# Optimization experiments

Measured on AMD Instinct MI355X. Metric: run time of the kernel, lower is better.

Reference implementation:

```python
import jax, jax.numpy as jnp
import numpy as np

TEMPERATURE = 1.0
EPS = 1e-12


def _l2_normalize(x, axis):
    # torch F.normalize: x / max(||x||_2, eps)
    n = jnp.sqrt(jnp.sum(x * x, axis=axis, keepdims=True))
    return x / jnp.maximum(n, EPS)


def setup_inputs() -> dict:
    key = jax.random.key(0)
    k1, k2 = jax.random.split(key)
    B, C, H, W = 2, 128, 128, 256
    K = 20
    features = jax.random.normal(k1, (B, C, H, W), dtype=jnp.float32)
    prototypes = jax.random.normal(k2, (K, C), dtype=jnp.float32)
    distance_scale = jnp.ones((1,), dtype=jnp.float32)
    return {"features": features, "prototypes": prototypes, "distance_scale": distance_scale}


def reference(features, prototypes, distance_scale):
    # features: [B, C, H, W] -> transpose(1,3) -> [B, W, H, C]
    f = jnp.transpose(features, (0, 3, 2, 1))
    # torch F.normalize default dim=1: on [B, W, H, C] this is the W axis (faithful)
    fn = _l2_normalize(f, axis=1)
    # prototypes [K, C], normalized along dim=1 (features)
    pn = _l2_normalize(prototypes, axis=1)
    # exact euclidean cdist (donot_use_mm): broadcasted diff [B, W, H, K, C]
    diff = fn[:, :, :, None, :] - pn[None, None, None, :, :]
    dist = jnp.sqrt(jnp.sum(diff * diff, axis=-1))  # [B, W, H, K]
    dist = jnp.abs(distance_scale) * dist
    # transpose(3,1): [B, K, H, W]
    logits = -jnp.transpose(dist, (0, 3, 2, 1))
    return logits / TEMPERATURE
```

## Files before the change

### kernel.cpp

```cpp
#include <hip/hip_runtime.h>
#include <math.h>

#define B 2
#define C 128
#define H 128
#define W 256
#define K 20

__global__ __launch_bounds__(256) void isomax_kernel(
    const float* __restrict__ feats,
    const float* __restrict__ protos,
    const float* __restrict__ dscale,
    float* __restrict__ out)
{
    __shared__ __align__(16) float s_pn[C * K];
    __shared__ float s_rn[C];
    __shared__ float s_rp[K];

    const int tid = threadIdx.x;
    const int bh  = blockIdx.x;
    const int b   = bh / H;
    const int h   = bh % H;

    if (tid < K) {
        float ss = 0.f;
        const float* p = protos + tid * C;
        for (int c = 0; c < C; ++c) { float v = p[c]; ss = fmaf(v, v, ss); }
        s_rp[tid] = 1.0f / fmaxf(sqrtf(ss), 1e-12f);
    }
    __syncthreads();

    for (int i = tid; i < K * C; i += 256) {
        int k = i >> 7;
        int c = i & (C - 1);
        s_pn[c * K + k] = protos[i] * s_rp[k];
    }

    const int wave = tid >> 6;
    const int lane = tid & 63;
    for (int c = wave; c < C; c += 4) {
        const float* row = feats + ((size_t)((b * C + c) * H + h)) * W;
        float4 v = ((const float4*)row)[lane];
        float ss = fmaf(v.x, v.x, fmaf(v.y, v.y, fmaf(v.z, v.z, v.w * v.w)));
        #pragma unroll
        for (int off = 32; off > 0; off >>= 1)
            ss += __shfl_xor(ss, off, 64);
        if (lane == 0) s_rn[c] = 1.0f / fmaxf(sqrtf(ss), 1e-12f);
    }
    __syncthreads();

    float acc[K];
    #pragma unroll
    for (int k = 0; k < K; ++k) acc[k] = 0.f;

    const float* fcol = feats + ((size_t)(b * C) * H + h) * W + tid;
    #pragma unroll 4
    for (int c = 0; c < C; ++c) {
        float v = fcol[(size_t)c * H * W] * s_rn[c];
        const float4* pn4 = (const float4*)(&s_pn[c * K]);
        #pragma unroll
        for (int q = 0; q < 5; ++q) {
            float4 p = pn4[q];
            float d0 = v - p.x; acc[q * 4 + 0] = fmaf(d0, d0, acc[q * 4 + 0]);
            float d1 = v - p.y; acc[q * 4 + 1] = fmaf(d1, d1, acc[q * 4 + 1]);
            float d2 = v - p.z; acc[q * 4 + 2] = fmaf(d2, d2, acc[q * 4 + 2]);
            float d3 = v - p.w; acc[q * 4 + 3] = fmaf(d3, d3, acc[q * 4 + 3]);
        }
    }

    const float scale = fabsf(dscale[0]);
    float* ob = out + ((size_t)(b * K) * H + h) * W + tid;
    #pragma unroll
    for (int k = 0; k < K; ++k) {
        ob[(size_t)k * H * W] = -scale * sqrtf(acc[k]);
    }
}

extern "C" void kernel_launch(void* const* d_in, const int* in_sizes, int n_in,
                              void* d_out, int out_size, void* d_ws, size_t ws_size,
                              hipStream_t stream) {
    const float* feats  = (const float*)d_in[0];
    const float* protos = (const float*)d_in[1];
    const float* dscale = (const float*)d_in[2];
    float* out = (float*)d_out;

    isomax_kernel<<<B * H, 256, 0, stream>>>(feats, protos, dscale, out);
}
```

Before: 106.8 us.

## Split W into halves and channels across waves with shared-memory reduction

Launches twice as many blocks, each of 512 threads covering half the W row. The channel loop is split into four chunks of 32 and the partial distance sums are reduced through shared memory before the sqrt and store. Prototype norms are now computed in parallel with wave shuffles instead of a serial loop over 20 threads. The aim is more parallelism and shorter serial chains on a small grid. The cost is that each block still recomputes the full per-channel row norms (reading all W) and the prototype normalization, plus extra LDS traffic and syncs.

```diff
diff --git a/kernel.cpp b/kernel.cpp
--- a/kernel.cpp
+++ b/kernel.cpp
@@ -6,8 +6,12 @@
 #define H 128
 #define W 256
 #define K 20
+#define NT 512
+#define WTILE 128
+#define NCCH 4
+#define CCH 32
 
-__global__ __launch_bounds__(256) void isomax_kernel(
+__global__ __launch_bounds__(NT, 4) void isomax_kernel(
     const float* __restrict__ feats,
     const float* __restrict__ protos,
     const float* __restrict__ dscale,
@@ -16,29 +20,28 @@
     __shared__ __align__(16) float s_pn[C * K];
     __shared__ float s_rn[C];
     __shared__ float s_rp[K];
+    __shared__ float s_red[NCCH][K][WTILE];
 
-    const int tid = threadIdx.x;
-    const int bh  = blockIdx.x;
-    const int b   = bh / H;
-    const int h   = bh % H;
+    const int tid   = threadIdx.x;
+    const int blk   = blockIdx.x;
+    const int whalf = blk & 1;
+    const int bh    = blk >> 1;
+    const int b     = bh / H;
+    const int h     = bh % H;
+    const int wave  = tid >> 6;
+    const int lane  = tid & 63;
 
-    if (tid < K) {
-        float ss = 0.f;
-        const float* p = protos + tid * C;
-        for (int c = 0; c < C; ++c) { float v = p[c]; ss = fmaf(v, v, ss); }
-        s_rp[tid] = 1.0f / fmaxf(sqrtf(ss), 1e-12f);
-    }
-    __syncthreads();
-
-    for (int i = tid; i < K * C; i += 256) {
-        int k = i >> 7;
-        int c = i & (C - 1);
-        s_pn[c * K + k] = protos[i] * s_rp[k];
+    for (int k = wave; k < K; k += 8) {
+        const float* p = protos + k * C;
+        float v0 = p[lane], v1 = p[lane + 64];
+        float ss = fmaf(v0, v0, v1 * v1);
+        #pragma unroll
+        for (int off = 32; off > 0; off >>= 1)
+            ss += __shfl_xor(ss, off, 64);
+        if (lane == 0) s_rp[k] = 1.0f / fmaxf(sqrtf(ss), 1e-12f);
     }
 
-    const int wave = tid >> 6;
-    const int lane = tid & 63;
-    for (int c = wave; c < C; c += 4) {
+    for (int c = wave; c < C; c += 8) {
         const float* row = feats + ((size_t)((b * C + c) * H + h)) * W;
         float4 v = ((const float4*)row)[lane];
         float ss = fmaf(v.x, v.x, fmaf(v.y, v.y, fmaf(v.z, v.z, v.w * v.w)));
@@ -49,14 +52,27 @@
     }
     __syncthreads();
 
+    for (int i = tid; i < K * C; i += NT) {
+        int k = i >> 7;
+        int c = i & (C - 1);
+        s_pn[c * K + k] = protos[i] * s_rp[k];
+    }
+    __syncthreads();
+
+    const int wl  = tid & (WTILE - 1);
+    const int cch = tid >> 7;
+    const int w   = whalf * WTILE + wl;
+
     float acc[K];
     #pragma unroll
     for (int k = 0; k < K; ++k) acc[k] = 0.f;
 
-    const float* fcol = feats + ((size_t)(b * C) * H + h) * W + tid;
+    const float* fcol = feats + ((size_t)(b * C) * H + h) * W + w;
+    const int c0 = cch * CCH;
     #pragma unroll 4
-    for (int c = 0; c < C; ++c) {
-        float v = fcol[(size_t)c * H * W] * s_rn[c];
+    for (int ci = 0; ci < CCH; ++ci) {
+        const int c = c0 + ci;
+        float v = fcol[(size_t)c * (H * W)] * s_rn[c];
         const float4* pn4 = (const float4*)(&s_pn[c * K]);
         #pragma unroll
         for (int q = 0; q < 5; ++q) {
@@ -68,11 +84,19 @@
         }
     }
 
+    #pragma unroll
+    for (int k = 0; k < K; ++k) s_red[cch][k][wl] = acc[k];
+    __syncthreads();
+
     const float scale = fabsf(dscale[0]);
-    float* ob = out + ((size_t)(b * K) * H + h) * W + tid;
+    const int ow = tid & (WTILE - 1);
+    const int kg = tid >> 7;
+    float* ob = out + ((size_t)(b * K) * H + h) * W + whalf * WTILE + ow;
     #pragma unroll
-    for (int k = 0; k < K; ++k) {
-        ob[(size_t)k * H * W] = -scale * sqrtf(acc[k]);
+    for (int j = 0; j < 5; ++j) {
+        const int k = kg * 5 + j;
+        float s = s_red[0][k][ow] + s_red[1][k][ow] + s_red[2][k][ow] + s_red[3][k][ow];
+        ob[(size_t)k * (H * W)] = -scale * sqrtf(s);
     }
 }
 
@@ -84,5 +108,5 @@
     const float* dscale = (const float*)d_in[2];
     float* out = (float*)d_out;
 
-    isomax_kernel<<<B * H, 256, 0, stream>>>(feats, protos, dscale, out);
+    isomax_kernel<<<B * H * 2, NT, 0, stream>>>(feats, protos, dscale, out);
 }
```

New measurement: 92.83 us. 13.1% less time.

## Split into prep and distance kernels using norm-expansion distance formula

Applied to the files above, without the earlier changes.

Replaces the direct squared-difference distance with the expansion ||v||^2 + ||p||^2 - 2 v·p, so each feature value costs one FMA per prototype plus one for its own norm. Row norms and normalized, regrouped prototypes are computed once in a separate prep kernel and kept in workspace. The distance kernel now splits the prototypes across the four waves (5 per wave) over 64-wide column tiles, so there are four times as many blocks. The costs are an extra launch, a second full read of the features, and cancellation error in the expanded form, which is clamped at zero.

```diff
diff --git a/kernel.cpp b/kernel.cpp
--- a/kernel.cpp
+++ b/kernel.cpp
@@ -6,73 +6,117 @@
 #define H 128
 #define W 256
 #define K 20
+#define HW (H * W)
 
-__global__ __launch_bounds__(256) void isomax_kernel(
-    const float* __restrict__ feats,
-    const float* __restrict__ protos,
-    const float* __restrict__ dscale,
-    float* __restrict__ out)
+__global__ __launch_bounds__(256) void isomax_prep(
+    const float* __restrict__ feats, const float* __restrict__ protos,
+    float* __restrict__ rn_ws, float* __restrict__ pn_ws, float* __restrict__ ppsum_ws)
 {
-    __shared__ __align__(16) float s_pn[C * K];
-    __shared__ float s_rn[C];
-    __shared__ float s_rp[K];
+    const int tid = threadIdx.x, wave = tid >> 6, lane = tid & 63;
+    const int blk = blockIdx.x;
 
-    const int tid = threadIdx.x;
-    const int bh  = blockIdx.x;
-    const int b   = bh / H;
-    const int h   = bh % H;
-
-    if (tid < K) {
-        float ss = 0.f;
-        const float* p = protos + tid * C;
-        for (int c = 0; c < C; ++c) { float v = p[c]; ss = fmaf(v, v, ss); }
-        s_rp[tid] = 1.0f / fmaxf(sqrtf(ss), 1e-12f);
-    }
-    __syncthreads();
-
-    for (int i = tid; i < K * C; i += 256) {
-        int k = i >> 7;
-        int c = i & (C - 1);
-        s_pn[c * K + k] = protos[i] * s_rp[k];
-    }
-
-    const int wave = tid >> 6;
-    const int lane = tid & 63;
-    for (int c = wave; c < C; c += 4) {
-        const float* row = feats + ((size_t)((b * C + c) * H + h)) * W;
-        float4 v = ((const float4*)row)[lane];
+    if (blk < 8192) {
+        const int r = blk * 4 + wave;
+        const float4 v = ((const float4*)(feats + (size_t)r * W))[lane];
         float ss = fmaf(v.x, v.x, fmaf(v.y, v.y, fmaf(v.z, v.z, v.w * v.w)));
         #pragma unroll
-        for (int off = 32; off > 0; off >>= 1)
-            ss += __shfl_xor(ss, off, 64);
-        if (lane == 0) s_rn[c] = 1.0f / fmaxf(sqrtf(ss), 1e-12f);
+        for (int off = 32; off > 0; off >>= 1) ss += __shfl_xor(ss, off, 64);
+        if (lane == 0) {
+            const int h  = r & (H - 1);
+            const int bc = r >> 7;
+            const int c  = bc & (C - 1);
+            const int b  = bc >> 7;
+            rn_ws[(b * H + h) * C + c] = 1.0f / fmaxf(sqrtf(ss), 1e-12f);
+        }
+    } else {
+        __shared__ float s_rp[32];
+        __shared__ float s_pp[32];
+        for (int k = wave; k < K; k += 4) {
+            const float* p = protos + k * C;
+            float a = p[lane], bq = p[lane + 64];
+            float ss = fmaf(a, a, bq * bq);
+            #pragma unroll
+            for (int off = 32; off > 0; off >>= 1) ss += __shfl_xor(ss, off, 64);
+            if (lane == 0) {
+                float n  = sqrtf(ss);
+                float rp = 1.0f / fmaxf(n, 1e-12f);
+                s_rp[k] = rp;
+                float nn = n * rp;
+                s_pp[k] = nn * nn;
+            }
+        }
+        __syncthreads();
+        for (int i = tid; i < C * K; i += 256) {
+            const int kg  = i / 640;
+            const int rem = i - kg * 640;
+            const int c   = rem / 5;
+            const int j   = rem - c * 5;
+            const int k   = kg * 5 + j;
+            pn_ws[i] = protos[k * C + c] * s_rp[k];
+        }
+        if (tid < K) ppsum_ws[tid] = s_pp[tid];
     }
-    __syncthreads();
+}
 
-    float acc[K];
-    #pragma unroll
-    for (int k = 0; k < K; ++k) acc[k] = 0.f;
+__global__ __launch_bounds__(256, 4) void isomax_dist(
+    const float* __restrict__ feats, const float* __restrict__ rn_ws,
+    const float* __restrict__ pn_ws, const float* __restrict__ ppsum_ws,
+    const float* __restrict__ dscale, float* __restrict__ out)
+{
+    const int tid = threadIdx.x;
+    const int kg  = __builtin_amdgcn_readfirstlane(tid >> 6);
+    const int wl  = tid & 63;
+    const int blk = blockIdx.x;
+    const int wt  = blk & 3;
+    const int bh  = blk >> 2;
+    const int b   = bh >> 7;
+    const int h   = bh & 127;
+    const int w   = wt * 64 + wl;
 
-    const float* fcol = feats + ((size_t)(b * C) * H + h) * W + tid;
+    const float* fp = feats + ((size_t)b * C * H + h) * W + w;
+    const float* rn = rn_ws + bh * C;
+    const float* pk = pn_ws + kg * (C * 5);
+
+    float S = 0.f;
+    float dacc[5] = {0.f, 0.f, 0.f, 0.f, 0.f};
+
     #pragma unroll 4
-    for (int c = 0; c < C; ++c) {
-        float v = fcol[(size_t)c * H * W] * s_rn[c];
-        const float4* pn4 = (const float4*)(&s_pn[c * K]);
+    for (int c0 = 0; c0 < C; c0 += 4) {
+        const float4 r4 = *(const float4*)(rn + c0);
+        float pp[20];
+        ((float4*)pp)[0] = *(const float4*)(pk + c0 * 5 + 0);
+        ((float4*)pp)[1] = *(const float4*)(pk + c0 * 5 + 4);
+        ((float4*)pp)[2] = *(const float4*)(pk + c0 * 5 + 8);
+        ((float4*)pp)[3] = *(const float4*)(pk + c0 * 5 + 12);
+        ((float4*)pp)[4] = *(const float4*)(pk + c0 * 5 + 16);
+
+        const float v0 = fp[(size_t)(c0 + 0) * HW] * r4.x;
+        const float v1 = fp[(size_t)(c0 + 1) * HW] * r4.y;
+        const float v2 = fp[(size_t)(c0 + 2) * HW] * r4.z;
+        const float v3 = fp[(size_t)(c0 + 3) * HW] * r4.w;
+        S = fmaf(v0, v0, S);
+        S = fmaf(v1, v1, S);
+        S = fmaf(v2, v2, S);
+        S = fmaf(v3, v3, S);
         #pragma unroll
-        for (int q = 0; q < 5; ++q) {
-            float4 p = pn4[q];
-            float d0 = v - p.x; acc[q * 4 + 0] = fmaf(d0, d0, acc[q * 4 + 0]);
-            float d1 = v - p.y; acc[q * 4 + 1] = fmaf(d1, d1, acc[q * 4 + 1]);
-            float d2 = v - p.z; acc[q * 4 + 2] = fmaf(d2, d2, acc[q * 4 + 2]);
-            float d3 = v - p.w; acc[q * 4 + 3] = fmaf(d3, d3, acc[q * 4 + 3]);
+        for (int j = 0; j < 5; ++j) {
+            float d = dacc[j];
+            d = fmaf(v0, pp[j],      d);
+            d = fmaf(v1, pp[5 + j],  d);
+            d = fmaf(v2, pp[10 + j], d);
+            d = fmaf(v3, pp[15 + j], d);
+            dacc[j] = d;
         }
     }
 
     const float scale = fabsf(dscale[0]);
-    float* ob = out + ((size_t)(b * K) * H + h) * W + tid;
+    const float* pps = ppsum_ws + kg * 5;
+    float* ob = out + ((size_t)b * K * H + h) * W + w;
     #pragma unroll
-    for (int k = 0; k < K; ++k) {
-        ob[(size_t)k * H * W] = -scale * sqrtf(acc[k]);
+    for (int j = 0; j < 5; ++j) {
+        const int k = kg * 5 + j;
+        float dist2 = fmaxf(fmaf(-2.f, dacc[j], S + pps[j]), 0.f);
+        ob[(size_t)k * HW] = -scale * sqrtf(dist2);
     }
 }
 
@@ -84,5 +128,11 @@
     const float* dscale = (const float*)d_in[2];
     float* out = (float*)d_out;
 
-    isomax_kernel<<<B * H, 256, 0, stream>>>(feats, protos, dscale, out);
+    float* rn_ws    = (float*)d_ws;
+    float* pn_ws    = rn_ws + 32768;
+    float* ppsum_ws = pn_ws + 2560;
+
+    isomax_prep<<<8193, 256, 0, stream>>>(feats, protos, rn_ws, pn_ws, ppsum_ws);
+    isomax_dist<<<B * H * (W / 64), 256, 0, stream>>>(feats, rn_ws, pn_ws, ppsum_ws,
+                                                      dscale, out);
 }
```

Result: faster. 96.91 us (-9.3%).

## Compute prototype distances via bf16 MFMA dot products with norm expansion

Applied to the files above, without the earlier changes.

Replaces the per-thread direct squared-difference accumulation with the expansion ||u||^2 + ||p||^2 - 2u·p. The dot products run on 16x16x32 bf16 MFMA instructions, and both norms are computed from the bf16-rounded values so the terms stay consistent. Blocks grow to 1024 threads, with 16 waves each taking 16 columns, and outputs are staged in shared memory for vectorized float4 stores. Quantizing to bf16 and using the expansion can introduce cancellation error and loses precision relative to the exact fp32 cdist.

```diff
diff --git a/kernel.cpp b/kernel.cpp
--- a/kernel.cpp
+++ b/kernel.cpp
@@ -6,73 +6,135 @@
 #define H 128
 #define W 256
 #define K 20
+#define HW (H * W)
+#define SO_STRIDE 260
 
-__global__ __launch_bounds__(256) void isomax_kernel(
-    const float* __restrict__ feats,
-    const float* __restrict__ protos,
-    const float* __restrict__ dscale,
-    float* __restrict__ out)
+typedef float f32x4 __attribute__((ext_vector_type(4)));
+typedef short bf16x8 __attribute__((ext_vector_type(8)));
+
+__device__ __forceinline__ unsigned f2bf_bits(float x) {
+    unsigned u = __float_as_uint(x);
+    return (u + 0x7FFFu + ((u >> 16) & 1u)) >> 16;
+}
+__device__ __forceinline__ float bf_to_f(unsigned bits) {
+    return __uint_as_float(bits << 16);
+}
+
+__global__ __launch_bounds__(1024) void isomax_fused(
+    const float* __restrict__ feats, const float* __restrict__ protos,
+    const float* __restrict__ dscale, float* __restrict__ out)
 {
-    __shared__ __align__(16) float s_pn[C * K];
     __shared__ float s_rn[C];
-    __shared__ float s_rp[K];
+    __shared__ float s_rp[32];
+    __shared__ float s_pp[32];
+    __shared__ float s_S[W];
+    __shared__ __align__(16) float s_o[K * SO_STRIDE];
 
-    const int tid = threadIdx.x;
-    const int bh  = blockIdx.x;
-    const int b   = bh / H;
-    const int h   = bh % H;
+    const int tid  = threadIdx.x;
+    const int wave = tid >> 6, lane = tid & 63;
+    const int quad = lane >> 4, l16 = lane & 15;
+    const int bh   = blockIdx.x;
+    const int b    = bh >> 7, h = bh & 127;
+    const int m0   = wave * 16;
 
-    if (tid < K) {
-        float ss = 0.f;
-        const float* p = protos + tid * C;
-        for (int c = 0; c < C; ++c) { float v = p[c]; ss = fmaf(v, v, ss); }
-        s_rp[tid] = 1.0f / fmaxf(sqrtf(ss), 1e-12f);
-    }
-    __syncthreads();
-
-    for (int i = tid; i < K * C; i += 256) {
-        int k = i >> 7;
-        int c = i & (C - 1);
-        s_pn[c * K + k] = protos[i] * s_rp[k];
+    #pragma unroll
+    for (int rd = 0; rd < 2; ++rd) {
+        const int k = rd * 16 + wave;
+        if (k < K) {
+            const float* p = protos + k * C;
+            const float a = p[lane], b2 = p[lane + 64];
+            float ss = fmaf(a, a, b2 * b2);
+            #pragma unroll
+            for (int off = 32; off > 0; off >>= 1) ss += __shfl_xor(ss, off, 64);
+            const float rp = 1.0f / fmaxf(sqrtf(ss), 1e-12f);
+            const float q0 = bf_to_f(f2bf_bits(a * rp));
+            const float q1 = bf_to_f(f2bf_bits(b2 * rp));
+            float s2 = fmaf(q0, q0, q1 * q1);
+            #pragma unroll
+            for (int off = 32; off > 0; off >>= 1) s2 += __shfl_xor(s2, off, 64);
+            if (lane == 0) { s_rp[k] = rp; s_pp[k] = s2; }
+        }
     }
 
-    const int wave = tid >> 6;
-    const int lane = tid & 63;
-    for (int c = wave; c < C; c += 4) {
+    for (int c = wave; c < C; c += 16) {
         const float* row = feats + ((size_t)((b * C + c) * H + h)) * W;
-        float4 v = ((const float4*)row)[lane];
+        const float4 v = ((const float4*)row)[lane];
         float ss = fmaf(v.x, v.x, fmaf(v.y, v.y, fmaf(v.z, v.z, v.w * v.w)));
         #pragma unroll
-        for (int off = 32; off > 0; off >>= 1)
-            ss += __shfl_xor(ss, off, 64);
+        for (int off = 32; off > 0; off >>= 1) ss += __shfl_xor(ss, off, 64);
         if (lane == 0) s_rn[c] = 1.0f / fmaxf(sqrtf(ss), 1e-12f);
     }
     __syncthreads();
 
-    float acc[K];
+    bf16x8 bfrag[4][2];
     #pragma unroll
-    for (int k = 0; k < K; ++k) acc[k] = 0.f;
-
-    const float* fcol = feats + ((size_t)(b * C) * H + h) * W + tid;
-    #pragma unroll 4
-    for (int c = 0; c < C; ++c) {
-        float v = fcol[(size_t)c * H * W] * s_rn[c];
-        const float4* pn4 = (const float4*)(&s_pn[c * K]);
+    for (int t = 0; t < 2; ++t) {
+        const int k = t * 16 + l16;
+        const float rp = (k < K) ? s_rp[k] : 0.0f;
         #pragma unroll
-        for (int q = 0; q < 5; ++q) {
-            float4 p = pn4[q];
-            float d0 = v - p.x; acc[q * 4 + 0] = fmaf(d0, d0, acc[q * 4 + 0]);
-            float d1 = v - p.y; acc[q * 4 + 1] = fmaf(d1, d1, acc[q * 4 + 1]);
-            float d2 = v - p.z; acc[q * 4 + 2] = fmaf(d2, d2, acc[q * 4 + 2]);
-            float d3 = v - p.w; acc[q * 4 + 3] = fmaf(d3, d3, acc[q * 4 + 3]);
+        for (int ch = 0; ch < 4; ++ch) {
+            bf16x8 f = {0, 0, 0, 0, 0, 0, 0, 0};
+            if (k < K) {
+                const float* pr = protos + k * C + ch * 32 + quad * 8;
+                const float4 pa = *(const float4*)(pr);
+                const float4 pb = *(const float4*)(pr + 4);
+                f[0] = (short)f2bf_bits(pa.x * rp);
+                f[1] = (short)f2bf_bits(pa.y * rp);
+                f[2] = (short)f2bf_bits(pa.z * rp);
+                f[3] = (short)f2bf_bits(pa.w * rp);
+                f[4] = (short)f2bf_bits(pb.x * rp);
+                f[5] = (short)f2bf_bits(pb.y * rp);
+                f[6] = (short)f2bf_bits(pb.z * rp);
+                f[7] = (short)f2bf_bits(pb.w * rp);
+            }
+            bfrag[ch][t] = f;
         }
     }
 
+    f32x4 acc0 = {0.f, 0.f, 0.f, 0.f}, acc1 = {0.f, 0.f, 0.f, 0.f};
+    float Sp = 0.f;
+    const float* fbase = feats + ((size_t)(b * C) * H + h) * W + m0 + l16;
+    #pragma unroll
+    for (int ch = 0; ch < 4; ++ch) {
+        bf16x8 af;
+        #pragma unroll
+        for (int j = 0; j < 8; ++j) {
+            const int c = ch * 32 + quad * 8 + j;
+            const float uf = fbase[(size_t)c * HW] * s_rn[c];
+            const unsigned bits = f2bf_bits(uf);
+            af[j] = (short)bits;
+            const float ur = bf_to_f(bits);
+            Sp = fmaf(ur, ur, Sp);
+        }
+        acc0 = __builtin_amdgcn_mfma_f32_16x16x32_bf16(af, bfrag[ch][0], acc0, 0, 0, 0);
+        acc1 = __builtin_amdgcn_mfma_f32_16x16x32_bf16(af, bfrag[ch][1], acc1, 0, 0, 0);
+    }
+
+    Sp += __shfl_xor(Sp, 16, 64);
+    Sp += __shfl_xor(Sp, 32, 64);
+    if (lane < 16) s_S[m0 + lane] = Sp;
+    __syncthreads();
+
     const float scale = fabsf(dscale[0]);
-    float* ob = out + ((size_t)(b * K) * H + h) * W + tid;
+    const float pcol0 = s_pp[l16];
+    const float pcol1 = (l16 < 4) ? s_pp[16 + l16] : 0.0f;
     #pragma unroll
-    for (int k = 0; k < K; ++k) {
-        ob[(size_t)k * H * W] = -scale * sqrtf(acc[k]);
+    for (int r = 0; r < 4; ++r) {
+        const int wl = m0 + quad * 4 + r;
+        const float Sm = s_S[wl];
+        const float d20 = fmaxf(Sm + pcol0 - 2.0f * acc0[r], 0.f);
+        s_o[l16 * SO_STRIDE + wl] = -scale * sqrtf(d20);
+        if (l16 < 4) {
+            const float d21 = fmaxf(Sm + pcol1 - 2.0f * acc1[r], 0.f);
+            s_o[(16 + l16) * SO_STRIDE + wl] = -scale * sqrtf(d21);
+        }
+    }
+    __syncthreads();
+
+    for (int i = tid; i < K * (W / 4); i += 1024) {
+        const int k = i >> 6, g = i & 63;
+        const float4 v = *(const float4*)&s_o[k * SO_STRIDE + g * 4];
+        *(float4*)(out + ((size_t)(b * K + k)) * HW + h * W + g * 4) = v;
     }
 }
 
@@ -84,5 +146,5 @@
     const float* dscale = (const float*)d_in[2];
     float* out = (float*)d_out;
 
-    isomax_kernel<<<B * H, 256, 0, stream>>>(feats, protos, dscale, out);
+    isomax_fused<<<B * H, 1024, 0, stream>>>(feats, protos, dscale, out);
 }
```

Result: faster. 86.82 us (-18.7%).
